# Optimization experiments

Hardware: AMD Instinct MI355X
Metric: run time of the kernel (lower is better)

Reference implementation:

```python
import jax, jax.numpy as jnp
import numpy as np

N_NODES = 50000
N_EDGES = 800000
D_FEAT = 32
J = 4
NUM_GRAPHS = 64
MAX_SCALE = 2 ** (J - 1)  # 8 diffusion steps


def _propagate(x, src, dst, w):
    # gather x_j, weight per-edge, scatter-add into target nodes
    msgs = x[src] * w[:, None]
    return jax.ops.segment_sum(msgs, dst, num_segments=N_NODES)


def _diffuse(x, src, dst, w):
    outs = []
    x_curr = x
    for step in range(1, MAX_SCALE + 1):
        x_curr = _propagate(x_curr, src, dst, w)
        if step & (step - 1) == 0:  # collect at powers of two: 1,2,4,8 -> J scales
            outs.append(x_curr)
    return outs


def setup_inputs() -> dict:
    key = jax.random.key(0)
    k1, k2, k3, k4 = jax.random.split(key, 4)
    X = jax.random.normal(k1, (N_NODES, D_FEAT), dtype=jnp.float32)
    edge_index = jax.random.randint(k2, (2, N_EDGES), 0, N_NODES, dtype=jnp.int64)
    edge_weight = jax.random.uniform(k3, (N_EDGES,), dtype=jnp.float32)
    batch = jnp.sort(jax.random.randint(k4, (N_NODES,), 0, NUM_GRAPHS, dtype=jnp.int64))
    return {"X": X, "edge_index": edge_index, "edge_weight": edge_weight, "batch": batch}


def reference(X, edge_index, edge_weight, batch):
    src, dst = edge_index[0], edge_index[1]
    diff_list = _diffuse(X, src, dst, edge_weight)
    # F0: deepest scale
    F0 = diff_list[-1]
    # F1: first-order wavelet coefficients |psi_j x|
    F1 = jnp.concatenate(
        [jnp.abs(diff_list[i - 1] - diff_list[i]) for i in range(1, len(diff_list))],
        axis=1,
    )
    # F2: second-order, diffuse concatenated scales once more
    U = jnp.concatenate(diff_list, axis=1)  # [N, J*d]
    U_diff = _diffuse(U, src, dst, edge_weight)
    res = []
    for j in range(J):
        cs, ce = j * D_FEAT, (j + 1) * D_FEAT
        for jp in range(j + 1, J):
            res.append(jnp.abs(U_diff[jp][:, cs:ce] - U_diff[jp - 1][:, cs:ce]))
    F2 = jnp.concatenate(res, axis=1)
    feats = jnp.concatenate([F0, F1, F2], axis=1)  # [N, d*(1 + (J-1) + J*(J-1)/2)] = [N, 320]
    # global_mean_pool over batch assignment
    sums = jax.ops.segment_sum(feats, batch, num_segments=NUM_GRAPHS)
    counts = jax.ops.segment_sum(jnp.ones((feats.shape[0],), feats.dtype), batch, num_segments=NUM_GRAPHS)
    return sums / jnp.maximum(counts, 1.0)[:, None]
```

## Files before the change

### kernel.cpp

```cpp
#include <hip/hip_runtime.h>

#define N_NODES 50000
#define N_EDGES 800000
#define D_FEAT 32
#define NUM_GRAPHS 64
#define FEATS 320
#define NBIN 128
#define BINSH 9
#define CE 4096
#define NCHUNK ((N_EDGES + CE - 1) / CE)
#define NPB ((N_NODES + 511) / 512)

__device__ __forceinline__ unsigned short f2bf(float f) {
    unsigned int u = __float_as_uint(f);
    u = (u + 0x7fffu + ((u >> 16) & 1u)) >> 16;
    return (unsigned short)u;
}
__device__ __forceinline__ float bf2f(unsigned short h) {
    return __uint_as_float((unsigned int)h << 16);
}


__global__ void hist_kernel(const int* __restrict__ dst, int* __restrict__ deg, int n) {
    int e = blockIdx.x * blockDim.x + threadIdx.x;
    if (e < n) atomicAdd(&deg[dst[e]], 1);
}

__global__ void scan1_kernel(const int* __restrict__ deg, int* __restrict__ inc,
                             int* __restrict__ blksum, int n) {
    __shared__ int s[1024];
    int t = threadIdx.x;
    int i = blockIdx.x * 1024 + t;
    int v = (i < n) ? deg[i] : 0;
    s[t] = v;
    __syncthreads();
    for (int off = 1; off < 1024; off <<= 1) {
        int u = (t >= off) ? s[t - off] : 0;
        __syncthreads();
        s[t] += u;
        __syncthreads();
    }
    if (i < n) inc[i] = s[t];
    if (t == 1023) blksum[blockIdx.x] = s[1023];
}

__global__ void scan2_kernel(const int* __restrict__ blksum, int* __restrict__ blkoff, int nblk) {
    __shared__ int s[64];
    int t = threadIdx.x;
    int v = (t < nblk) ? blksum[t] : 0;
    s[t] = v;
    __syncthreads();
    for (int off = 1; off < 64; off <<= 1) {
        int u = (t >= off) ? s[t - off] : 0;
        __syncthreads();
        s[t] += u;
        __syncthreads();
    }
    if (t < nblk) blkoff[t] = s[t] - v;
}

__global__ void scan3_kernel(const int* __restrict__ deg, const int* __restrict__ inc,
                             const int* __restrict__ blkoff, int* __restrict__ rowptr,
                             int n, int nedges) {
    int i = blockIdx.x * blockDim.x + threadIdx.x;
    if (i < n) rowptr[i] = inc[i] - deg[i] + blkoff[i >> 10];
    if (i == 0) rowptr[n] = nedges;
}


__global__ void binA_kernel(const int* __restrict__ dst, int* __restrict__ counts, int n) {
    __shared__ int h[NBIN];
    int t = threadIdx.x;
    if (t < NBIN) h[t] = 0;
    __syncthreads();
    int s0 = blockIdx.x * CE, e0 = min(s0 + CE, n);
    for (int i = s0 + t; i < e0; i += blockDim.x)
        atomicAdd(&h[dst[i] >> BINSH], 1);
    __syncthreads();
    if (t < NBIN) counts[blockIdx.x * NBIN + t] = h[t];
}

__global__ void binB_kernel(const int* __restrict__ rowptr, int* __restrict__ counts, int n) {
    int bin = threadIdx.x;
    int node0 = bin << BINSH;
    int running = rowptr[min(node0, n)];
    for (int c = 0; c < NCHUNK; ++c) {
        int idx = c * NBIN + bin;
        int v = counts[idx];
        counts[idx] = running;
        running += v;
    }
}

__global__ __launch_bounds__(256) void binC_kernel(const int* __restrict__ src,
                                                   const int* __restrict__ dst,
                                                   const float* __restrict__ w,
                                                   const int* __restrict__ counts,
                                                   int2* __restrict__ tmp, int n) {
    __shared__ int h[NBIN], sc[NBIN], cur[NBIN], gbase[NBIN];
    __shared__ int2 srec[CE];
    __shared__ unsigned char sbin[CE];
    int t = threadIdx.x;
    if (t < NBIN) h[t] = 0;
    __syncthreads();
    int s0 = blockIdx.x * CE, e0 = min(s0 + CE, n);
    int cnt = e0 - s0;
    for (int i = s0 + t; i < e0; i += blockDim.x)
        atomicAdd(&h[dst[i] >> BINSH], 1);
    __syncthreads();
    if (t < NBIN) sc[t] = h[t];
    __syncthreads();
    for (int off = 1; off < NBIN; off <<= 1) {
        int u = (t < NBIN && t >= off) ? sc[t - off] : 0;
        __syncthreads();
        if (t < NBIN) sc[t] += u;
        __syncthreads();
    }
    if (t < NBIN) {
        cur[t] = 0;
        gbase[t] = counts[blockIdx.x * NBIN + t];
    }
    __syncthreads();
    for (int i = s0 + t; i < e0; i += blockDim.x) {
        int d = dst[i];
        int b = d >> BINSH;
        int pos = (sc[b] - h[b]) + atomicAdd(&cur[b], 1);
        srec[pos] = make_int2(src[i] | ((int)f2bf(w[i]) << 16), d & 511);
        sbin[pos] = (unsigned char)b;
    }
    __syncthreads();
    for (int j = t; j < cnt; j += blockDim.x) {
        int b = sbin[j];
        tmp[gbase[b] + (j - (sc[b] - h[b]))] = srec[j];
    }
}

__global__ void place_kernel(const int* __restrict__ rowptr, const int2* __restrict__ tmp,
                             unsigned int* __restrict__ edges, int n) {
    __shared__ int rp[513];
    __shared__ int cur[512];
    int node0 = blockIdx.x << BINSH;
    int t = threadIdx.x;
    for (int i = t; i <= 512; i += blockDim.x) rp[i] = rowptr[min(node0 + i, n)];
    for (int i = t; i < 512; i += blockDim.x) cur[i] = 0;
    __syncthreads();
    int e0 = rp[0], e1 = rp[512];
    for (int e = e0 + t; e < e1; e += blockDim.x) {
        int2 p = tmp[e];
        int pos = rp[p.y] + atomicAdd(&cur[p.y], 1);
        edges[pos] = (unsigned int)p.x;
    }
}


__global__ void cvt_kernel(const float4* __restrict__ xin, ushort4* __restrict__ xout, int n4) {
    int i = blockIdx.x * blockDim.x + threadIdx.x;
    if (i < n4) {
        float4 v = xin[i];
        ushort4 o;
        o.x = f2bf(v.x); o.y = f2bf(v.y); o.z = f2bf(v.z); o.w = f2bf(v.w);
        xout[i] = o;
    }
}


__global__ void gbound_kernel(const int* __restrict__ batch, int* __restrict__ gstart, int n) {
    int i = blockIdx.x * blockDim.x + threadIdx.x;
    if (i >= n) return;
    int g = batch[i];
    int gp = (i == 0) ? -1 : batch[i - 1];
    for (int gg = gp + 1; gg <= g; ++gg) gstart[gg] = i;
    if (i == n - 1)
        for (int gg = g + 1; gg <= NUM_GRAPHS; ++gg) gstart[gg] = n;
}


__global__ void spmm_kernel(const ushort4* __restrict__ xin,
                            ushort4* __restrict__ yout,
                            const int* __restrict__ rowptr,
                            const unsigned int* __restrict__ edges, int n) {
    int lane = threadIdx.x & 7;
    int node = (blockIdx.x * blockDim.x + threadIdx.x) >> 3;
    if (node >= n) return;
    int e0 = rowptr[node], e1 = rowptr[node + 1];
    float a0 = 0.f, a1 = 0.f, a2 = 0.f, a3 = 0.f;
    int e = e0;
    int e4 = e0 + ((e1 - e0) & ~3);
    for (; e < e4; e += 4) {
        unsigned int r0 = edges[e + 0];
        unsigned int r1 = edges[e + 1];
        unsigned int r2 = edges[e + 2];
        unsigned int r3 = edges[e + 3];
        ushort4 v0 = xin[(size_t)(r0 & 0xffff) * 8 + lane];
        ushort4 v1 = xin[(size_t)(r1 & 0xffff) * 8 + lane];
        ushort4 v2 = xin[(size_t)(r2 & 0xffff) * 8 + lane];
        ushort4 v3 = xin[(size_t)(r3 & 0xffff) * 8 + lane];
        float w0 = bf2f((unsigned short)(r0 >> 16));
        float w1 = bf2f((unsigned short)(r1 >> 16));
        float w2 = bf2f((unsigned short)(r2 >> 16));
        float w3 = bf2f((unsigned short)(r3 >> 16));
        a0 += bf2f(v0.x) * w0; a1 += bf2f(v0.y) * w0; a2 += bf2f(v0.z) * w0; a3 += bf2f(v0.w) * w0;
        a0 += bf2f(v1.x) * w1; a1 += bf2f(v1.y) * w1; a2 += bf2f(v1.z) * w1; a3 += bf2f(v1.w) * w1;
        a0 += bf2f(v2.x) * w2; a1 += bf2f(v2.y) * w2; a2 += bf2f(v2.z) * w2; a3 += bf2f(v2.w) * w2;
        a0 += bf2f(v3.x) * w3; a1 += bf2f(v3.y) * w3; a2 += bf2f(v3.z) * w3; a3 += bf2f(v3.w) * w3;
    }
    for (; e < e1; ++e) {
        unsigned int r = edges[e];
        ushort4 v = xin[(size_t)(r & 0xffff) * 8 + lane];
        float w = bf2f((unsigned short)(r >> 16));
        a0 += bf2f(v.x) * w; a1 += bf2f(v.y) * w; a2 += bf2f(v.z) * w; a3 += bf2f(v.w) * w;
    }
    yout[(size_t)node * 8 + lane] = make_ushort4(f2bf(a0), f2bf(a1), f2bf(a2), f2bf(a3));
}


struct PoolArgs10 {
    const unsigned short* P[10];
    const unsigned short* Q[10];
};

__global__ __launch_bounds__(320) void pool_kernel(PoolArgs10 a, const int* __restrict__ gstart,
                                                   float* __restrict__ out) {
    int k = threadIdx.x >> 5;
    int f = threadIdx.x & 31;
    int g = blockIdx.x >> 4;
    int s = blockIdx.x & 15;
    int gs = gstart[g], ge = gstart[g + 1];
    int len = ge - gs;
    int i0 = gs + ((len * s) >> 4);
    int i1 = gs + ((len * (s + 1)) >> 4);
    const unsigned short* __restrict__ P = a.P[k];
    const unsigned short* __restrict__ Q = a.Q[k];
    float acc = 0.f;
    if (Q) {
        for (int i = i0; i < i1; ++i)
            acc += fabsf(bf2f(P[(size_t)i * 32 + f]) - bf2f(Q[(size_t)i * 32 + f]));
    } else {
        for (int i = i0; i < i1; ++i)
            acc += bf2f(P[(size_t)i * 32 + f]);
    }
    if (i1 > i0) atomicAdd(&out[g * FEATS + k * 32 + f], acc);
}

__global__ void divide_kernel(float* __restrict__ out, const int* __restrict__ gstart, int total) {
    int i = blockIdx.x * blockDim.x + threadIdx.x;
    if (i < total) {
        int g = i / FEATS;
        float c = (float)(gstart[g + 1] - gstart[g]);
        out[i] /= fmaxf(c, 1.0f);
    }
}


extern "C" void kernel_launch(void* const* d_in, const int* in_sizes, int n_in,
                              void* d_out, int out_size, void* d_ws, size_t ws_size,
                              hipStream_t stream) {
    const float* X     = (const float*)d_in[0];
    const int*   ei    = (const int*)d_in[1];
    const float* ew    = (const float*)d_in[2];
    const int*   batch = (const int*)d_in[3];
    float* out = (float*)d_out;

    const int N = N_NODES, E = N_EDGES;
    const int* src = ei;
    const int* dst = ei + E;

    char* base = (char*)d_ws;
    size_t off = 0;
    auto alloc = [&](size_t bytes) -> void* {
        void* p = base + off;
        off += (bytes + 255) & ~(size_t)255;
        return p;
    };
    unsigned short* y[13];
    for (int k = 0; k <= 12; ++k) y[k] = (unsigned short*)alloc((size_t)N * 32 * 2);

    int*  deg    = (int*)alloc((size_t)N * 4);
    int*  inc    = (int*)alloc((size_t)N * 4);
    int*  rowptr = (int*)alloc((size_t)(N + 4) * 4);
    int*  blksum = (int*)alloc(64 * 4);
    int*  blkoff = (int*)alloc(64 * 4);
    int*  gstart = (int*)alloc((NUM_GRAPHS + 1) * 4);
    int*  counts = (int*)alloc((size_t)NCHUNK * NBIN * 4);
    int2* tmp    = (int2*)alloc((size_t)E * 8);
    unsigned int* edges = (unsigned int*)alloc((size_t)E * 4);

    hipMemsetAsync(deg, 0, (size_t)N * 4, stream);
    hipMemsetAsync(out, 0, (size_t)out_size * 4, stream);

    hist_kernel<<<(E + 255) / 256, 256, 0, stream>>>(dst, deg, E);
    const int NBLK = (N + 1023) / 1024;
    scan1_kernel<<<NBLK, 1024, 0, stream>>>(deg, inc, blksum, N);
    scan2_kernel<<<1, 64, 0, stream>>>(blksum, blkoff, NBLK);
    scan3_kernel<<<(N + 255) / 256, 256, 0, stream>>>(deg, inc, blkoff, rowptr, N, E);

    binA_kernel<<<NCHUNK, 256, 0, stream>>>(dst, counts, E);
    binB_kernel<<<1, NBIN, 0, stream>>>(rowptr, counts, N);
    binC_kernel<<<NCHUNK, 256, 0, stream>>>(src, dst, ew, counts, tmp, E);
    place_kernel<<<NPB, 256, 0, stream>>>(rowptr, tmp, edges, N);

    cvt_kernel<<<(N * 32 / 4 + 255) / 256, 256, 0, stream>>>((const float4*)X, (ushort4*)y[0],
                                                             N * 32 / 4);
    gbound_kernel<<<(N + 255) / 256, 256, 0, stream>>>(batch, gstart, N);

    const int SPMM_GRID = (N * 8 + 255) / 256;
    for (int k = 1; k <= 12; ++k) {
        spmm_kernel<<<SPMM_GRID, 256, 0, stream>>>((const ushort4*)y[k - 1], (ushort4*)y[k],
                                                   rowptr, edges, N);
    }

    {
        PoolArgs10 p{};
        const unsigned short* Ps[10] = {y[8], y[1], y[2], y[4], y[3], y[5], y[9], y[6], y[10], y[12]};
        const unsigned short* Qs[10] = {nullptr, y[2], y[4], y[8], y[2], y[3], y[5], y[4], y[6], y[8]};
        for (int k = 0; k < 10; ++k) { p.P[k] = Ps[k]; p.Q[k] = Qs[k]; }
        pool_kernel<<<NUM_GRAPHS * 16, 320, 0, stream>>>(p, gstart, out);
    }

    divide_kernel<<<(out_size + 255) / 256, 256, 0, stream>>>(out, gstart, out_size);
}
```

Baseline: 317.6 us.

## Derive CSR rowptr inside bin/place kernels; unroll SpMM edge loop by eight

Removes the separate degree histogram and three-pass scan, so the row pointers are built from the bin counts instead. binB now sums and scans the per-bin totals, and place_kernel builds a local per-node histogram and scan to write rowptr and place edges. This cuts four kernel launches, a memset and a pass over dst. The SpMM inner loop is also unrolled to eight gathers in flight per iteration, which may raise register pressure.

```diff
diff --git a/kernel.cpp b/kernel.cpp
--- a/kernel.cpp
+++ b/kernel.cpp
@@ -21,53 +21,6 @@
 }
 
 
-__global__ void hist_kernel(const int* __restrict__ dst, int* __restrict__ deg, int n) {
-    int e = blockIdx.x * blockDim.x + threadIdx.x;
-    if (e < n) atomicAdd(&deg[dst[e]], 1);
-}
-
-__global__ void scan1_kernel(const int* __restrict__ deg, int* __restrict__ inc,
-                             int* __restrict__ blksum, int n) {
-    __shared__ int s[1024];
-    int t = threadIdx.x;
-    int i = blockIdx.x * 1024 + t;
-    int v = (i < n) ? deg[i] : 0;
-    s[t] = v;
-    __syncthreads();
-    for (int off = 1; off < 1024; off <<= 1) {
-        int u = (t >= off) ? s[t - off] : 0;
-        __syncthreads();
-        s[t] += u;
-        __syncthreads();
-    }
-    if (i < n) inc[i] = s[t];
-    if (t == 1023) blksum[blockIdx.x] = s[1023];
-}
-
-__global__ void scan2_kernel(const int* __restrict__ blksum, int* __restrict__ blkoff, int nblk) {
-    __shared__ int s[64];
-    int t = threadIdx.x;
-    int v = (t < nblk) ? blksum[t] : 0;
-    s[t] = v;
-    __syncthreads();
-    for (int off = 1; off < 64; off <<= 1) {
-        int u = (t >= off) ? s[t - off] : 0;
-        __syncthreads();
-        s[t] += u;
-        __syncthreads();
-    }
-    if (t < nblk) blkoff[t] = s[t] - v;
-}
-
-__global__ void scan3_kernel(const int* __restrict__ deg, const int* __restrict__ inc,
-                             const int* __restrict__ blkoff, int* __restrict__ rowptr,
-                             int n, int nedges) {
-    int i = blockIdx.x * blockDim.x + threadIdx.x;
-    if (i < n) rowptr[i] = inc[i] - deg[i] + blkoff[i >> 10];
-    if (i == 0) rowptr[n] = nedges;
-}
-
-
 __global__ void binA_kernel(const int* __restrict__ dst, int* __restrict__ counts, int n) {
     __shared__ int h[NBIN];
     int t = threadIdx.x;
@@ -80,12 +33,27 @@
     if (t < NBIN) counts[blockIdx.x * NBIN + t] = h[t];
 }
 
-__global__ void binB_kernel(const int* __restrict__ rowptr, int* __restrict__ counts, int n) {
-    int bin = threadIdx.x;
-    int node0 = bin << BINSH;
-    int running = rowptr[min(node0, n)];
+__global__ void binB_kernel(int* __restrict__ counts, int* __restrict__ binBase) {
+    __shared__ int s[NBIN];
+    int b = threadIdx.x;
+    int tot = 0;
+    #pragma unroll 8
+    for (int c = 0; c < NCHUNK; ++c) tot += counts[c * NBIN + b];
+    s[b] = tot;
+    __syncthreads();
+    for (int off = 1; off < NBIN; off <<= 1) {
+        int u = (b >= off) ? s[b - off] : 0;
+        __syncthreads();
+        s[b] += u;
+        __syncthreads();
+    }
+    int base = s[b] - tot;
+    binBase[b] = base;
+    if (b == NBIN - 1) binBase[NBIN] = s[b];
+    int running = base;
+    #pragma unroll 4
     for (int c = 0; c < NCHUNK; ++c) {
-        int idx = c * NBIN + bin;
+        int idx = c * NBIN + b;
         int v = counts[idx];
         counts[idx] = running;
         running += v;
@@ -135,19 +103,41 @@
     }
 }
 
-__global__ void place_kernel(const int* __restrict__ rowptr, const int2* __restrict__ tmp,
-                             unsigned int* __restrict__ edges, int n) {
-    __shared__ int rp[513];
-    __shared__ int cur[512];
-    int node0 = blockIdx.x << BINSH;
+__global__ __launch_bounds__(256) void place_kernel(const int* __restrict__ binBase,
+                                                    const int2* __restrict__ tmp,
+                                                    unsigned int* __restrict__ edges,
+                                                    int* __restrict__ rowptr, int n) {
+    __shared__ int h[512], sc[512], cur[512];
+    int b = blockIdx.x;
     int t = threadIdx.x;
-    for (int i = t; i <= 512; i += blockDim.x) rp[i] = rowptr[min(node0 + i, n)];
-    for (int i = t; i < 512; i += blockDim.x) cur[i] = 0;
-    __syncthreads();
-    int e0 = rp[0], e1 = rp[512];
-    for (int e = e0 + t; e < e1; e += blockDim.x) {
+    int base = binBase[b], end = binBase[b + 1];
+    for (int i = t; i < 512; i += 256) { h[i] = 0; cur[i] = 0; }
+    __syncthreads();
+    for (int e = base + t; e < end; e += 256)
+        atomicAdd(&h[tmp[e].y], 1);
+    __syncthreads();
+    for (int i = t; i < 512; i += 256) sc[i] = h[i];
+    __syncthreads();
+    for (int off = 1; off < 512; off <<= 1) {
+        int i0 = t, i1 = t + 256;
+        int a0 = (i0 >= off) ? sc[i0 - off] : 0;
+        int a1 = (i1 >= off) ? sc[i1 - off] : 0;
+        __syncthreads();
+        sc[i0] += a0;
+        sc[i1] += a1;
+        __syncthreads();
+    }
+    int node0 = b << BINSH;
+    for (int i = t; i < 512; i += 256) {
+        int node = node0 + i;
+        if (node <= n) rowptr[node] = base + sc[i] - h[i];
+    }
+    if (b == 0 && t == 0) rowptr[0] = 0;
+    __syncthreads();
+    for (int e = base + t; e < end; e += 256) {
         int2 p = tmp[e];
-        int pos = rp[p.y] + atomicAdd(&cur[p.y], 1);
+        int loc = p.y;
+        int pos = base + (sc[loc] - h[loc]) + atomicAdd(&cur[loc], 1);
         edges[pos] = (unsigned int)p.x;
     }
 }
@@ -175,34 +165,34 @@
 }
 
 
-__global__ void spmm_kernel(const ushort4* __restrict__ xin,
-                            ushort4* __restrict__ yout,
-                            const int* __restrict__ rowptr,
-                            const unsigned int* __restrict__ edges, int n) {
+__global__ __launch_bounds__(256) void spmm_kernel(const ushort4* __restrict__ xin,
+                                                   ushort4* __restrict__ yout,
+                                                   const int* __restrict__ rowptr,
+                                                   const unsigned int* __restrict__ edges,
+                                                   int n) {
     int lane = threadIdx.x & 7;
     int node = (blockIdx.x * blockDim.x + threadIdx.x) >> 3;
     if (node >= n) return;
     int e0 = rowptr[node], e1 = rowptr[node + 1];
     float a0 = 0.f, a1 = 0.f, a2 = 0.f, a3 = 0.f;
     int e = e0;
-    int e4 = e0 + ((e1 - e0) & ~3);
-    for (; e < e4; e += 4) {
-        unsigned int r0 = edges[e + 0];
-        unsigned int r1 = edges[e + 1];
-        unsigned int r2 = edges[e + 2];
-        unsigned int r3 = edges[e + 3];
-        ushort4 v0 = xin[(size_t)(r0 & 0xffff) * 8 + lane];
-        ushort4 v1 = xin[(size_t)(r1 & 0xffff) * 8 + lane];
-        ushort4 v2 = xin[(size_t)(r2 & 0xffff) * 8 + lane];
-        ushort4 v3 = xin[(size_t)(r3 & 0xffff) * 8 + lane];
-        float w0 = bf2f((unsigned short)(r0 >> 16));
-        float w1 = bf2f((unsigned short)(r1 >> 16));
-        float w2 = bf2f((unsigned short)(r2 >> 16));
-        float w3 = bf2f((unsigned short)(r3 >> 16));
-        a0 += bf2f(v0.x) * w0; a1 += bf2f(v0.y) * w0; a2 += bf2f(v0.z) * w0; a3 += bf2f(v0.w) * w0;
-        a0 += bf2f(v1.x) * w1; a1 += bf2f(v1.y) * w1; a2 += bf2f(v1.z) * w1; a3 += bf2f(v1.w) * w1;
-        a0 += bf2f(v2.x) * w2; a1 += bf2f(v2.y) * w2; a2 += bf2f(v2.z) * w2; a3 += bf2f(v2.w) * w2;
-        a0 += bf2f(v3.x) * w3; a1 += bf2f(v3.y) * w3; a2 += bf2f(v3.z) * w3; a3 += bf2f(v3.w) * w3;
+    int e8 = e0 + ((e1 - e0) & ~7);
+    for (; e < e8; e += 8) {
+        unsigned int r[8];
+        #pragma unroll
+        for (int u = 0; u < 8; ++u) r[u] = edges[e + u];
+        ushort4 v[8];
+        #pragma unroll
+        for (int u = 0; u < 8; ++u)
+            v[u] = xin[(size_t)(r[u] & 0xffff) * 8 + lane];
+        #pragma unroll
+        for (int u = 0; u < 8; ++u) {
+            float w = bf2f((unsigned short)(r[u] >> 16));
+            a0 += bf2f(v[u].x) * w;
+            a1 += bf2f(v[u].y) * w;
+            a2 += bf2f(v[u].z) * w;
+            a3 += bf2f(v[u].w) * w;
+        }
     }
     for (; e < e1; ++e) {
         unsigned int r = edges[e];
@@ -275,29 +265,19 @@
     unsigned short* y[13];
     for (int k = 0; k <= 12; ++k) y[k] = (unsigned short*)alloc((size_t)N * 32 * 2);
 
-    int*  deg    = (int*)alloc((size_t)N * 4);
-    int*  inc    = (int*)alloc((size_t)N * 4);
-    int*  rowptr = (int*)alloc((size_t)(N + 4) * 4);
-    int*  blksum = (int*)alloc(64 * 4);
-    int*  blkoff = (int*)alloc(64 * 4);
-    int*  gstart = (int*)alloc((NUM_GRAPHS + 1) * 4);
-    int*  counts = (int*)alloc((size_t)NCHUNK * NBIN * 4);
-    int2* tmp    = (int2*)alloc((size_t)E * 8);
+    int*  rowptr  = (int*)alloc((size_t)(N + 4) * 4);
+    int*  gstart  = (int*)alloc((NUM_GRAPHS + 1) * 4);
+    int*  counts  = (int*)alloc((size_t)NCHUNK * NBIN * 4);
+    int*  binBase = (int*)alloc((NBIN + 1) * 4);
+    int2* tmp     = (int2*)alloc((size_t)E * 8);
     unsigned int* edges = (unsigned int*)alloc((size_t)E * 4);
 
-    hipMemsetAsync(deg, 0, (size_t)N * 4, stream);
     hipMemsetAsync(out, 0, (size_t)out_size * 4, stream);
 
-    hist_kernel<<<(E + 255) / 256, 256, 0, stream>>>(dst, deg, E);
-    const int NBLK = (N + 1023) / 1024;
-    scan1_kernel<<<NBLK, 1024, 0, stream>>>(deg, inc, blksum, N);
-    scan2_kernel<<<1, 64, 0, stream>>>(blksum, blkoff, NBLK);
-    scan3_kernel<<<(N + 255) / 256, 256, 0, stream>>>(deg, inc, blkoff, rowptr, N, E);
-
     binA_kernel<<<NCHUNK, 256, 0, stream>>>(dst, counts, E);
-    binB_kernel<<<1, NBIN, 0, stream>>>(rowptr, counts, N);
+    binB_kernel<<<1, NBIN, 0, stream>>>(counts, binBase);
     binC_kernel<<<NCHUNK, 256, 0, stream>>>(src, dst, ew, counts, tmp, E);
-    place_kernel<<<NPB, 256, 0, stream>>>(rowptr, tmp, edges, N);
+    place_kernel<<<NPB, 256, 0, stream>>>(binBase, tmp, edges, rowptr, N);
 
     cvt_kernel<<<(N * 32 / 4 + 255) / 256, 256, 0, stream>>>((const float4*)X, (ushort4*)y[0],
                                                              N * 32 / 4);
```

Result: faster. 294.5 us (-7.3%).
